# Kernel tuning notes

Measured on AMD Instinct MI355X. Metric: run time of the kernel, lower is better.

The kernel has to match this reference:

```python
import jax, jax.numpy as jnp
import numpy as np

N_CLASSES = 4
N_STEPS = 10
THRESHOLD = 0.7
ALPHA = 2.0


def _make_kernel_bias(n_classes, threshold):
    cross = np.zeros((3, 3, 3), dtype=np.float32)
    cross[1, 1, :] = 1.0
    cross[1, :, 1] = 1.0
    cross[:, 1, 1] = 1.0
    # depthwise kernel, OIDHW with I = 1 (groups = n_classes)
    kernel = (1.0 / 7.0 / (1.0 - threshold)) * np.tile(cross[None, None], (n_classes, 1, 1, 1, 1))
    bias = np.full((n_classes,), -threshold / (1.0 - threshold), dtype=np.float32)
    return jnp.asarray(kernel), jnp.asarray(bias)


def setup_inputs() -> dict:
    key = jax.random.key(0)
    k1, k2, k3 = jax.random.split(key, 3)
    B, C, D, H, W = 2, N_CLASSES, 128, 128, 128
    inp = jax.random.normal(k1, (B, C, D, H, W), dtype=jnp.float32)
    target = jax.random.randint(k2, (B, D, H, W), 0, C, dtype=jnp.int64)
    weight = jax.random.uniform(k3, (B, C), dtype=jnp.float32)
    kernel, bias = _make_kernel_bias(C, THRESHOLD)
    return {"input": inp, "target": target, "weight": weight, "kernel": kernel, "bias": bias}


def _erode(op, kernel, bias, n_classes):
    y = jax.lax.conv_general_dilated(
        op, kernel, window_strides=(1, 1, 1), padding=[(1, 1)] * 3,
        dimension_numbers=("NCDHW", "OIDHW", "NCDHW"),
        feature_group_count=n_classes)
    return jnp.maximum(y + bias[None, :, None, None, None], 0.0)


def reference(input, target, weight, kernel, bias):
    C = N_CLASSES
    probs = jax.nn.softmax(input, axis=1)
    # one_hot -> [B, D, H, W, C] -> [B, C, D, H, W]
    tgt = jnp.transpose(jax.nn.one_hot(target, C, dtype=probs.dtype), (0, 4, 1, 2, 3))
    op = jnp.square(probs - tgt)
    loss_t = jnp.zeros_like(op)
    for k in range(N_STEPS):
        op = _erode(op, kernel, bias, C)
        loss_t = loss_t + (float(k + 1) ** ALPHA) * op
    loss_t = loss_t * weight[:, :, None, None, None]
    return jnp.mean(loss_t)
```

## Files before the change

kernel.cpp:

```cpp
#include <hip/hip_runtime.h>

#define DHW   (128*128*128)
#define CDHW  (4*DHW)
#define NTOT  (2*CDHW)
#define NACC  1024

#define ROW4     32
#define IN_ROWS  12
#define S1_ROWS  10
#define IN_P4    (IN_ROWS*ROW4)
#define S1_P4    (S1_ROWS*ROW4)
#define SLOT4(z) (((z)+8)&3)
#define SLOT2(z) (((z)+8)&1)


__global__ __launch_bounds__(256, 4) void fused_sm_erode2_kernel(
    const float* __restrict__ in, const int* __restrict__ tgt,
    float4* __restrict__ dst,
    const float* __restrict__ kern, const float* __restrict__ bias,
    const float* __restrict__ weight, float c1, float c2,
    double* __restrict__ accs, int* __restrict__ flagOut)
{
    __shared__ float4 lin[4 * IN_P4];
    __shared__ float4 ls1[2 * S1_P4];
    __shared__ double wsum[4];
    __shared__ int    snz;

    const int tid = threadIdx.x;
    const int x  = blockIdx.x & 7;
    const int q  = blockIdx.x >> 3;
    const int c  = q & 3;
    const int t  = x * 32 + (q >> 2);
    const int y0 = (t & 15) << 3;
    const int zb = ((t >> 4) & 7) << 4;
    const int b  = (t >> 7) & 1;
    const int bc = b * 4 + c;
    const int fid = (bc << 7) | (((t >> 4) & 7) << 4) | (t & 15);

    const float4* in4 = (const float4*)in;
    const int4*   tg4 = (const int4*)tgt;
    const size_t  chb = ((size_t)(b * 4)) << 19;
    const size_t  co0 = chb + ((size_t)c << 19);
    const size_t  co1 = chb + ((size_t)((c + 1) & 3) << 19);
    const size_t  co2 = chb + ((size_t)((c + 2) & 3) << 19);
    const size_t  co3 = chb + ((size_t)((c + 3) & 3) << 19);
    float4*       dp  = dst + ((size_t)bc << 19);
    const float wk = kern[13];
    const float bs = bias[c];

    const int col  = tid & 31;
    const int trow = tid >> 5;

    if (tid == 0) snz = 0;

    const int  gy0  = y0 + trow - 2;
    const bool lv0  = ((unsigned)gy0 < 128u);
    const int  off0 = (lv0 ? gy0 : 0) * 32 + col;
    const bool act1 = (tid < 128);
    const int  gy1  = y0 + trow + 6;
    const bool lv1  = act1 && ((unsigned)gy1 < 128u);
    const int  off1 = (lv1 ? gy1 : 0) * 32 + col;

    const bool  sact1 = (tid < 64);
    const int   sr  = (tid < 32) ? 0 : 9;
    const float m1  = ((unsigned)(y0 + sr - 1) < 128u) ? 1.f : 0.f;
    const int   ci1 = (sr + 1) * 32 + (tid & 31);
    const int   so1 = sr * 32 + (tid & 31);

    const float lmask = (col == 0)  ? 0.f : 1.f;
    const float rmask = (col == 31) ? 0.f : 1.f;

    const int go4 = (y0 + trow) * 32 + col;

    const float4 f4z = make_float4(0.f, 0.f, 0.f, 0.f);
    float4 A00 = f4z, A01 = f4z, A02 = f4z, A03 = f4z;
    float4 A10 = f4z, A11 = f4z, A12 = f4z, A13 = f4z;
    int4   T0 = make_int4(0,0,0,0), T1 = make_int4(0,0,0,0);
    bool   ok0 = false, ok1 = false;
    float4 s_m = f4z, s_c = f4z, s_p = f4z;
    int    nz  = 0;

    auto prefetch = [&](int L) {
        const bool zok = ((unsigned)L < 128u);
        ok0 = zok && lv0;
        ok1 = zok && lv1;
        if (ok0) {
            size_t o = (size_t)(L << 12) + off0;
            A00 = in4[co0 + o];
            A01 = in4[co1 + o];
            A02 = in4[co2 + o];
            A03 = in4[co3 + o];
            T0  = tg4[((size_t)b << 19) + o];
        }
        if (ok1) {
            size_t o = (size_t)(L << 12) + off1;
            A10 = in4[co0 + o];
            A11 = in4[co1 + o];
            A12 = in4[co2 + o];
            A13 = in4[co3 + o];
            T1  = tg4[((size_t)b << 19) + o];
        }
    };
    auto op_one = [&](const float4& B0, const float4& B1, const float4& B2,
                      const float4& B3, const int4& T) -> float4 {
        float4 r;
        #define OP1(K)                                                         \
        {                                                                      \
            float vc = B0.K;                                                   \
            float sm = 1.0f + __expf(B1.K - vc) + __expf(B2.K - vc)            \
                            + __expf(B3.K - vc);                               \
            float d  = __builtin_amdgcn_rcpf(sm) - ((T.K == c) ? 1.0f : 0.0f); \
            r.K = d * d;                                                       \
        }
        OP1(x) OP1(y) OP1(z) OP1(w)
        #undef OP1
        return r;
    };
    auto commit = [&](int L) {
        float4* sl = lin + SLOT4(L) * IN_P4;
        float4 v0 = f4z, v1 = f4z;
        if (ok0) v0 = op_one(A00, A01, A02, A03, T0);
        if (ok1) v1 = op_one(A10, A11, A12, A13, T1);
        sl[tid] = v0;
        if (act1) sl[256 + tid] = v1;
    };
    auto s1one = [&](const float4* pzm, const float4* pzc, const float4* pzp,
                     int ci, float ym) -> float4 {
        float4 qC = pzc[ci];
        float4 qU = pzc[ci - 32];
        float4 qD = pzc[ci + 32];
        float4 qm = pzm[ci];
        float4 qp = pzp[ci];
        float lf = __shfl_up(qC.w, 1, 64)   * lmask;
        float rt = __shfl_down(qC.x, 1, 64) * rmask;
        float4 v;
        v.x = fmaxf((qC.x + lf   + qC.y + qU.x + qD.x + qm.x + qp.x) * wk + bs, 0.f) * ym;
        v.y = fmaxf((qC.y + qC.x + qC.z + qU.y + qD.y + qm.y + qp.y) * wk + bs, 0.f) * ym;
        v.z = fmaxf((qC.z + qC.y + qC.w + qU.z + qD.z + qm.z + qp.z) * wk + bs, 0.f) * ym;
        v.w = fmaxf((qC.w + qC.z + rt   + qU.w + qD.w + qm.w + qp.w) * wk + bs, 0.f) * ym;
        return v;
    };
    auto s1_phase = [&](int z) {
        float4* o = ls1 + SLOT2(z) * S1_P4;
        float4 vnew;
        if ((unsigned)z < 128u) {
            const float4* pzm = lin + SLOT4(z - 1) * IN_P4;
            const float4* pzc = lin + SLOT4(z)     * IN_P4;
            const float4* pzp = lin + SLOT4(z + 1) * IN_P4;
            vnew = s1one(pzm, pzc, pzp, tid + 64, 1.f);
            o[tid + 32] = vnew;
            if (sact1) o[so1] = s1one(pzm, pzc, pzp, ci1, m1);
        } else {
            vnew = f4z;
            o[tid + 32] = f4z;
            if (sact1) o[so1] = f4z;
        }
        s_m = s_c; s_c = s_p; s_p = vnew;
    };

    double part = 0.0;

    prefetch(zb - 2); commit(zb - 2);
    prefetch(zb - 1); commit(zb - 1);
    prefetch(zb);     commit(zb);
    prefetch(zb + 1);
    __syncthreads();
    s1_phase(zb - 1);

    for (int L = zb + 1; L <= zb + 17; ++L) {
        commit(L);
        __syncthreads();
        if (L <= zb + 16) prefetch(L + 1);
        s1_phase(L - 1);
        const int zo = L - 2;
        if (zo >= zb) {
            const float4* su = ls1 + SLOT2(zo) * S1_P4;
            float4 u4 = su[tid];
            float4 d4 = su[tid + 64];
            float lf = __shfl_up(s_c.w, 1, 64)   * lmask;
            float rt = __shfl_down(s_c.x, 1, 64) * rmask;
            float4 v;
            v.x = fmaxf((s_c.x + lf    + s_c.y + u4.x + d4.x + s_m.x + s_p.x) * wk + bs, 0.f);
            v.y = fmaxf((s_c.y + s_c.x + s_c.z + u4.y + d4.y + s_m.y + s_p.y) * wk + bs, 0.f);
            v.z = fmaxf((s_c.z + s_c.y + s_c.w + u4.z + d4.z + s_m.z + s_p.z) * wk + bs, 0.f);
            v.w = fmaxf((s_c.w + s_c.z + rt    + u4.w + d4.w + s_m.w + s_p.w) * wk + bs, 0.f);
            dp[((size_t)zo << 12) + go4] = v;
            nz |= (v.x != 0.f) | (v.y != 0.f) | (v.z != 0.f) | (v.w != 0.f);
            float pl = c1 * (s_c.x + s_c.y + s_c.z + s_c.w)
                     + c2 * (v.x   + v.y   + v.z   + v.w);
            part += (double)pl;
        }
    }

    #pragma unroll
    for (int off = 32; off > 0; off >>= 1)
        part += __shfl_down(part, off, 64);
    if ((tid & 63) == 0) wsum[tid >> 6] = part;
    if (__any(nz) && (tid & 63) == 0) atomicOr(&snz, 1);
    __syncthreads();
    if (tid == 0) {
        double tot = (wsum[0] + wsum[1] + wsum[2] + wsum[3]) * (double)weight[bc];
        accs[blockIdx.x] = tot;
        flagOut[fid] = snz;
    }
}

__global__ __launch_bounds__(256, 4) void erode2_kernel(
    const float4* __restrict__ src, float4* __restrict__ dst,
    const float* __restrict__ kern, const float* __restrict__ bias,
    const float* __restrict__ weight, float c1, float c2,
    int store, double* __restrict__ accs,
    const int* __restrict__ flagIn, int* __restrict__ flagOut)
{
    __shared__ float4 lin[4 * IN_P4];
    __shared__ float4 ls1[2 * S1_P4];
    __shared__ double wsum[4];
    __shared__ int    sf[9];
    __shared__ int    snz;

    const int tid = threadIdx.x;
    const int bid = ((blockIdx.x & 7) << 7) | (blockIdx.x >> 3);
    const int ty = bid & 15;
    const int tz = (bid >> 4) & 7;
    const int y0 = ty << 3;
    const int zb = tz << 4;
    const int bc = bid >> 7;

    if (tid < 9) {
        int dy = tid % 3 - 1, dz = tid / 3 - 1;
        int yt = ty + dy, zt = tz + dz;
        int f = 0;
        if ((unsigned)yt < 16u && (unsigned)zt < 8u)
            f = flagIn[(bc << 7) | (zt << 4) | yt];
        sf[tid] = f;
    }
    if (tid == 0) snz = 0;
    __syncthreads();
    const int any = sf[0] | sf[1] | sf[2] | sf[3] | sf[4]
                  | sf[5] | sf[6] | sf[7] | sf[8];
    if (!any) {
        if (tid == 0) {
            flagOut[bid] = 0;
        }
        return;
    }

    const float4* sp = src + ((size_t)bc << 19);
    float4*       dp = dst + ((size_t)bc << 19);
    const float wk = kern[13];
    const float bs = bias[bc & 3];

    const int col  = tid & 31;
    const int trow = tid >> 5;

    const int  gy0  = y0 + trow - 2;
    const bool lv0  = ((unsigned)gy0 < 128u);
    const int  off0 = (lv0 ? gy0 : 0) * 32 + col;
    const bool act1 = (tid < 128);
    const int  gy1  = y0 + trow + 6;
    const bool lv1  = act1 && ((unsigned)gy1 < 128u);
    const int  off1 = (lv1 ? gy1 : 0) * 32 + col;

    const int yd0 = (gy0 >> 3) - ty + 1;
    const int yd1 = (gy1 >> 3) - ty + 1;
    const int fmask0 = (sf[0 + ((unsigned)yd0 < 3u ? yd0 : 1)] ? 1 : 0)
                     | (sf[3 + ((unsigned)yd0 < 3u ? yd0 : 1)] ? 2 : 0)
                     | (sf[6 + ((unsigned)yd0 < 3u ? yd0 : 1)] ? 4 : 0);
    const int fmask1 = (sf[0 + ((unsigned)yd1 < 3u ? yd1 : 1)] ? 1 : 0)
                     | (sf[3 + ((unsigned)yd1 < 3u ? yd1 : 1)] ? 2 : 0)
                     | (sf[6 + ((unsigned)yd1 < 3u ? yd1 : 1)] ? 4 : 0);

    const bool  sact1 = (tid < 64);
    const int   sr  = (tid < 32) ? 0 : 9;
    const float m1  = ((unsigned)(y0 + sr - 1) < 128u) ? 1.f : 0.f;
    const int   ci1 = (sr + 1) * 32 + (tid & 31);
    const int   so1 = sr * 32 + (tid & 31);

    const float lmask = (col == 0)  ? 0.f : 1.f;
    const float rmask = (col == 31) ? 0.f : 1.f;

    const int go4 = (y0 + trow) * 32 + col;

    const float4 f4z = make_float4(0.f, 0.f, 0.f, 0.f);
    float4 pf0 = f4z, pf1 = f4z;
    float4 s_m = f4z, s_c = f4z, s_p = f4z;
    int    nz  = 0;

    auto prefetch = [&](int L) {
        pf0 = f4z; pf1 = f4z;
        if ((unsigned)L < 128u) {
            const int zidx = (L >> 4) - tz + 1;
            const float4* zp = sp + ((size_t)L << 12);
            if (lv0 && ((fmask0 >> zidx) & 1)) pf0 = zp[off0];
            if (lv1 && ((fmask1 >> zidx) & 1)) pf1 = zp[off1];
        }
    };
    auto commit = [&](int L) {
        float4* sl = lin + SLOT4(L) * IN_P4;
        sl[tid] = pf0;
        if (act1) sl[256 + tid] = pf1;
    };
    auto s1one = [&](const float4* pzm, const float4* pzc, const float4* pzp,
                     int ci, float ym) -> float4 {
        float4 qC = pzc[ci];
        float4 qU = pzc[ci - 32];
        float4 qD = pzc[ci + 32];
        float4 qm = pzm[ci];
        float4 qp = pzp[ci];
        float lf = __shfl_up(qC.w, 1, 64)   * lmask;
        float rt = __shfl_down(qC.x, 1, 64) * rmask;
        float4 v;
        v.x = fmaxf((qC.x + lf   + qC.y + qU.x + qD.x + qm.x + qp.x) * wk + bs, 0.f) * ym;
        v.y = fmaxf((qC.y + qC.x + qC.z + qU.y + qD.y + qm.y + qp.y) * wk + bs, 0.f) * ym;
        v.z = fmaxf((qC.z + qC.y + qC.w + qU.z + qD.z + qm.z + qp.z) * wk + bs, 0.f) * ym;
        v.w = fmaxf((qC.w + qC.z + rt   + qU.w + qD.w + qm.w + qp.w) * wk + bs, 0.f) * ym;
        return v;
    };
    auto s1_phase = [&](int z) {
        float4* o = ls1 + SLOT2(z) * S1_P4;
        float4 vnew;
        if ((unsigned)z < 128u) {
            const float4* pzm = lin + SLOT4(z - 1) * IN_P4;
            const float4* pzc = lin + SLOT4(z)     * IN_P4;
            const float4* pzp = lin + SLOT4(z + 1) * IN_P4;
            vnew = s1one(pzm, pzc, pzp, tid + 64, 1.f);
            o[tid + 32] = vnew;
            if (sact1) o[so1] = s1one(pzm, pzc, pzp, ci1, m1);
        } else {
            vnew = f4z;
            o[tid + 32] = f4z;
            if (sact1) o[so1] = f4z;
        }
        s_m = s_c; s_c = s_p; s_p = vnew;
    };

    double part = 0.0;

    prefetch(zb - 2); commit(zb - 2);
    prefetch(zb - 1); commit(zb - 1);
    prefetch(zb);     commit(zb);
    prefetch(zb + 1);
    __syncthreads();
    s1_phase(zb - 1);

    for (int L = zb + 1; L <= zb + 17; ++L) {
        commit(L);
        __syncthreads();
        if (L <= zb + 16) prefetch(L + 1);
        s1_phase(L - 1);
        const int zo = L - 2;
        if (zo >= zb) {
            const float4* su = ls1 + SLOT2(zo) * S1_P4;
            float4 u4 = su[tid];
            float4 d4 = su[tid + 64];
            float lf = __shfl_up(s_c.w, 1, 64)   * lmask;
            float rt = __shfl_down(s_c.x, 1, 64) * rmask;
            float4 v;
            v.x = fmaxf((s_c.x + lf    + s_c.y + u4.x + d4.x + s_m.x + s_p.x) * wk + bs, 0.f);
            v.y = fmaxf((s_c.y + s_c.x + s_c.z + u4.y + d4.y + s_m.y + s_p.y) * wk + bs, 0.f);
            v.z = fmaxf((s_c.z + s_c.y + s_c.w + u4.z + d4.z + s_m.z + s_p.z) * wk + bs, 0.f);
            v.w = fmaxf((s_c.w + s_c.z + rt    + u4.w + d4.w + s_m.w + s_p.w) * wk + bs, 0.f);
            if (store) dp[((size_t)zo << 12) + go4] = v;
            nz |= (v.x != 0.f) | (v.y != 0.f) | (v.z != 0.f) | (v.w != 0.f);
            float pl = c1 * (s_c.x + s_c.y + s_c.z + s_c.w)
                     + c2 * (v.x   + v.y   + v.z   + v.w);
            part += (double)pl;
        }
    }

    #pragma unroll
    for (int off = 32; off > 0; off >>= 1)
        part += __shfl_down(part, off, 64);
    if ((tid & 63) == 0) wsum[tid >> 6] = part;
    if (__any(nz) && (tid & 63) == 0) atomicOr(&snz, 1);
    __syncthreads();
    if (tid == 0) {
        flagOut[bid] = snz;
        double tot = (wsum[0] + wsum[1] + wsum[2] + wsum[3]) * (double)weight[bc];
        atomicAdd(&accs[bid], tot);
    }
}

__global__ __launch_bounds__(1024) void finalize_kernel(
    const double* __restrict__ accs, float* __restrict__ out)
{
    __shared__ double wsum[16];
    double v = accs[threadIdx.x];
    #pragma unroll
    for (int off = 32; off > 0; off >>= 1)
        v += __shfl_down(v, off, 64);
    int lane = threadIdx.x & 63;
    int wid  = threadIdx.x >> 6;
    if (lane == 0) wsum[wid] = v;
    __syncthreads();
    if (threadIdx.x == 0) {
        double tot = 0.0;
        #pragma unroll
        for (int i = 0; i < 16; ++i) tot += wsum[i];
        out[0] = (float)(tot / (double)NTOT);
    }
}

extern "C" void kernel_launch(void* const* d_in, const int* in_sizes, int n_in,
                              void* d_out, int out_size, void* d_ws, size_t ws_size,
                              hipStream_t stream) {
    const float* in     = (const float*)d_in[0];
    const int*   tgt    = (const int*)d_in[1];
    const float* weight = (const float*)d_in[2];
    const float* kern   = (const float*)d_in[3];
    const float* bias   = (const float*)d_in[4];
    float* out = (float*)d_out;

    char* ws = (char*)d_ws;
    float*  buf0   = (float*)ws;
    float*  buf1   = (float*)(ws + (size_t)NTOT * sizeof(float));
    double* accs   = (double*)(ws + (size_t)NTOT * 2 * sizeof(float));
    int*    flagsA = (int*)(ws + (size_t)NTOT * 2 * sizeof(float) + NACC * sizeof(double));
    int*    flagsB = flagsA + NACC;

    fused_sm_erode2_kernel<<<1024, 256, 0, stream>>>(
        in, tgt, (float4*)buf0, kern, bias, weight, 1.0f, 4.0f, accs, flagsA);

    float* cur = buf0;
    float* nxt = buf1;
    int*   fIn = flagsA;
    int*   fOut = flagsB;
    for (int p = 1; p < 5; ++p) {
        float c1 = (float)((2 * p + 1) * (2 * p + 1));
        float c2 = (float)((2 * p + 2) * (2 * p + 2));
        int   store = (p < 4) ? 1 : 0;
        erode2_kernel<<<1024, 256, 0, stream>>>(
            (const float4*)cur, (float4*)nxt, kern, bias, weight, c1, c2,
            store, accs, fIn, fOut);
        float* tb = cur; cur = nxt; nxt = tb;
        int*   tf = fIn; fIn = fOut; fOut = tf;
    }

    finalize_kernel<<<1, 1024, 0, stream>>>(accs, out);
}
```

Measured before the change: 163.6 us.

## Track per-z-slice nonzero flags to skip zero slice loads, compute and stores

Replaces the single per-tile nonzero flag with a 16-bit mask of z-slices that contain nonzero eroded values. Later erosion steps use the masks from neighbouring tiles to skip global loads, first-stage stencil work and second-stage compute for slices that must be zero. Stores are delayed by one iteration so that only slices voted nonzero get written. This adds per-slice ballot/atomic traffic and extra bit logic, and it relies on zero slices never being read back from stale memory.

```diff
diff --git a/kernel.cpp b/kernel.cpp
--- a/kernel.cpp
+++ b/kernel.cpp
@@ -24,7 +24,7 @@
     __shared__ float4 lin[4 * IN_P4];
     __shared__ float4 ls1[2 * S1_P4];
     __shared__ double wsum[4];
-    __shared__ int    snz;
+    __shared__ int    voteArr[16];
 
     const int tid = threadIdx.x;
     const int x  = blockIdx.x & 7;
@@ -51,7 +51,7 @@
     const int col  = tid & 31;
     const int trow = tid >> 5;
 
-    if (tid == 0) snz = 0;
+    if (tid < 16) voteArr[tid] = 0;
 
     const int  gy0  = y0 + trow - 2;
     const bool lv0  = ((unsigned)gy0 < 128u);
@@ -78,7 +78,7 @@
     int4   T0 = make_int4(0,0,0,0), T1 = make_int4(0,0,0,0);
     bool   ok0 = false, ok1 = false;
     float4 s_m = f4z, s_c = f4z, s_p = f4z;
-    int    nz  = 0;
+    float4 vH  = f4z;
 
     auto prefetch = [&](int L) {
         const bool zok = ((unsigned)L < 128u);
@@ -170,6 +170,9 @@
     for (int L = zb + 1; L <= zb + 17; ++L) {
         commit(L);
         __syncthreads();
+        const int zp = L - 3;
+        if (zp >= zb && voteArr[zp - zb] != 0)
+            dp[((size_t)zp << 12) + go4] = vH;
         if (L <= zb + 16) prefetch(L + 1);
         s1_phase(L - 1);
         const int zo = L - 2;
@@ -184,24 +187,30 @@
             v.y = fmaxf((s_c.y + s_c.x + s_c.z + u4.y + d4.y + s_m.y + s_p.y) * wk + bs, 0.f);
             v.z = fmaxf((s_c.z + s_c.y + s_c.w + u4.z + d4.z + s_m.z + s_p.z) * wk + bs, 0.f);
             v.w = fmaxf((s_c.w + s_c.z + rt    + u4.w + d4.w + s_m.w + s_p.w) * wk + bs, 0.f);
-            dp[((size_t)zo << 12) + go4] = v;
-            nz |= (v.x != 0.f) | (v.y != 0.f) | (v.z != 0.f) | (v.w != 0.f);
             float pl = c1 * (s_c.x + s_c.y + s_c.z + s_c.w)
                      + c2 * (v.x   + v.y   + v.z   + v.w);
             part += (double)pl;
-        }
-    }
+            bool nzv = (v.x != 0.f) || (v.y != 0.f) || (v.z != 0.f) || (v.w != 0.f);
+            if (__any(nzv) && (tid & 63) == 0) atomicOr(&voteArr[zo - zb], 1);
+            vH = v;
+        }
+    }
+
+    __syncthreads();
+    if (voteArr[15] != 0) dp[((size_t)(zb + 15) << 12) + go4] = vH;
 
     #pragma unroll
     for (int off = 32; off > 0; off >>= 1)
         part += __shfl_down(part, off, 64);
     if ((tid & 63) == 0) wsum[tid >> 6] = part;
-    if (__any(nz) && (tid & 63) == 0) atomicOr(&snz, 1);
     __syncthreads();
     if (tid == 0) {
+        int mask = 0;
+        #pragma unroll
+        for (int i = 0; i < 16; ++i) mask |= (voteArr[i] ? 1 : 0) << i;
+        flagOut[fid] = mask;
         double tot = (wsum[0] + wsum[1] + wsum[2] + wsum[3]) * (double)weight[bc];
         accs[blockIdx.x] = tot;
-        flagOut[fid] = snz;
     }
 }
 
@@ -216,7 +225,7 @@
     __shared__ float4 ls1[2 * S1_P4];
     __shared__ double wsum[4];
     __shared__ int    sf[9];
-    __shared__ int    snz;
+    __shared__ int    voteArr[16];
 
     const int tid = threadIdx.x;
     const int bid = ((blockIdx.x & 7) << 7) | (blockIdx.x >> 3);
@@ -234,16 +243,25 @@
             f = flagIn[(bc << 7) | (zt << 4) | yt];
         sf[tid] = f;
     }
-    if (tid == 0) snz = 0;
-    __syncthreads();
-    const int any = sf[0] | sf[1] | sf[2] | sf[3] | sf[4]
-                  | sf[5] | sf[6] | sf[7] | sf[8];
-    if (!any) {
-        if (tid == 0) {
-            flagOut[bid] = 0;
-        }
+    if (tid < 16) voteArr[tid] = 0;
+    __syncthreads();
+
+    unsigned aInW = 0;
+    #pragma unroll
+    for (int i = 0; i < 20; ++i) {
+        int L = zb - 2 + i;
+        if ((unsigned)L < 128u) {
+            int zi = (L >> 4) - tz + 1;
+            int m  = sf[zi * 3] | sf[zi * 3 + 1] | sf[zi * 3 + 2];
+            aInW |= (unsigned)((m >> (L & 15)) & 1) << i;
+        }
+    }
+    if (aInW == 0) {
+        if (tid == 0) flagOut[bid] = 0;
         return;
     }
+    const unsigned aS1W = aInW | (aInW << 1) | (aInW >> 1);
+    const unsigned aS2W = aS1W | (aS1W << 1) | (aS1W >> 1);
 
     const float4* sp = src + ((size_t)bc << 19);
     float4*       dp = dst + ((size_t)bc << 19);
@@ -261,14 +279,8 @@
     const bool lv1  = act1 && ((unsigned)gy1 < 128u);
     const int  off1 = (lv1 ? gy1 : 0) * 32 + col;
 
-    const int yd0 = (gy0 >> 3) - ty + 1;
-    const int yd1 = (gy1 >> 3) - ty + 1;
-    const int fmask0 = (sf[0 + ((unsigned)yd0 < 3u ? yd0 : 1)] ? 1 : 0)
-                     | (sf[3 + ((unsigned)yd0 < 3u ? yd0 : 1)] ? 2 : 0)
-                     | (sf[6 + ((unsigned)yd0 < 3u ? yd0 : 1)] ? 4 : 0);
-    const int fmask1 = (sf[0 + ((unsigned)yd1 < 3u ? yd1 : 1)] ? 1 : 0)
-                     | (sf[3 + ((unsigned)yd1 < 3u ? yd1 : 1)] ? 2 : 0)
-                     | (sf[6 + ((unsigned)yd1 < 3u ? yd1 : 1)] ? 4 : 0);
+    const int yd0c = (unsigned)((gy0 >> 3) - ty + 1) < 3u ? ((gy0 >> 3) - ty + 1) : 1;
+    const int yd1c = (unsigned)((gy1 >> 3) - ty + 1) < 3u ? ((gy1 >> 3) - ty + 1) : 1;
 
     const bool  sact1 = (tid < 64);
     const int   sr  = (tid < 32) ? 0 : 9;
@@ -284,15 +296,16 @@
     const float4 f4z = make_float4(0.f, 0.f, 0.f, 0.f);
     float4 pf0 = f4z, pf1 = f4z;
     float4 s_m = f4z, s_c = f4z, s_p = f4z;
-    int    nz  = 0;
+    float4 vH  = f4z;
 
     auto prefetch = [&](int L) {
         pf0 = f4z; pf1 = f4z;
         if ((unsigned)L < 128u) {
-            const int zidx = (L >> 4) - tz + 1;
+            const int zi = (L >> 4) - tz + 1;
+            const int sh = L & 15;
             const float4* zp = sp + ((size_t)L << 12);
-            if (lv0 && ((fmask0 >> zidx) & 1)) pf0 = zp[off0];
-            if (lv1 && ((fmask1 >> zidx) & 1)) pf1 = zp[off1];
+            if (lv0 && ((sf[zi * 3 + yd0c] >> sh) & 1)) pf0 = zp[off0];
+            if (lv1 && ((sf[zi * 3 + yd1c] >> sh) & 1)) pf1 = zp[off1];
         }
     };
     auto commit = [&](int L) {
@@ -317,19 +330,15 @@
         return v;
     };
     auto s1_phase = [&](int z) {
-        float4* o = ls1 + SLOT2(z) * S1_P4;
-        float4 vnew;
-        if ((unsigned)z < 128u) {
+        float4 vnew = f4z;
+        if ((unsigned)z < 128u && ((aS1W >> (z - zb + 2)) & 1)) {
+            float4* o = ls1 + SLOT2(z) * S1_P4;
             const float4* pzm = lin + SLOT4(z - 1) * IN_P4;
             const float4* pzc = lin + SLOT4(z)     * IN_P4;
             const float4* pzp = lin + SLOT4(z + 1) * IN_P4;
             vnew = s1one(pzm, pzc, pzp, tid + 64, 1.f);
             o[tid + 32] = vnew;
             if (sact1) o[so1] = s1one(pzm, pzc, pzp, ci1, m1);
-        } else {
-            vnew = f4z;
-            o[tid + 32] = f4z;
-            if (sact1) o[so1] = f4z;
         }
         s_m = s_c; s_c = s_p; s_p = vnew;
     };
@@ -346,36 +355,50 @@
     for (int L = zb + 1; L <= zb + 17; ++L) {
         commit(L);
         __syncthreads();
+        const int zp = L - 3;
+        if (store && zp >= zb && voteArr[zp - zb] != 0)
+            dp[((size_t)zp << 12) + go4] = vH;
         if (L <= zb + 16) prefetch(L + 1);
         s1_phase(L - 1);
         const int zo = L - 2;
         if (zo >= zb) {
-            const float4* su = ls1 + SLOT2(zo) * S1_P4;
-            float4 u4 = su[tid];
-            float4 d4 = su[tid + 64];
-            float lf = __shfl_up(s_c.w, 1, 64)   * lmask;
-            float rt = __shfl_down(s_c.x, 1, 64) * rmask;
-            float4 v;
-            v.x = fmaxf((s_c.x + lf    + s_c.y + u4.x + d4.x + s_m.x + s_p.x) * wk + bs, 0.f);
-            v.y = fmaxf((s_c.y + s_c.x + s_c.z + u4.y + d4.y + s_m.y + s_p.y) * wk + bs, 0.f);
-            v.z = fmaxf((s_c.z + s_c.y + s_c.w + u4.z + d4.z + s_m.z + s_p.z) * wk + bs, 0.f);
-            v.w = fmaxf((s_c.w + s_c.z + rt    + u4.w + d4.w + s_m.w + s_p.w) * wk + bs, 0.f);
-            if (store) dp[((size_t)zo << 12) + go4] = v;
-            nz |= (v.x != 0.f) | (v.y != 0.f) | (v.z != 0.f) | (v.w != 0.f);
-            float pl = c1 * (s_c.x + s_c.y + s_c.z + s_c.w)
-                     + c2 * (v.x   + v.y   + v.z   + v.w);
-            part += (double)pl;
-        }
-    }
+            float4 v = f4z;
+            if ((aS2W >> (zo - zb + 2)) & 1) {
+                float4 u4 = f4z, d4 = f4z;
+                if ((aS1W >> (zo - zb + 2)) & 1) {
+                    const float4* su = ls1 + SLOT2(zo) * S1_P4;
+                    u4 = su[tid];
+                    d4 = su[tid + 64];
+                }
+                float lf = __shfl_up(s_c.w, 1, 64)   * lmask;
+                float rt = __shfl_down(s_c.x, 1, 64) * rmask;
+                v.x = fmaxf((s_c.x + lf    + s_c.y + u4.x + d4.x + s_m.x + s_p.x) * wk + bs, 0.f);
+                v.y = fmaxf((s_c.y + s_c.x + s_c.z + u4.y + d4.y + s_m.y + s_p.y) * wk + bs, 0.f);
+                v.z = fmaxf((s_c.z + s_c.y + s_c.w + u4.z + d4.z + s_m.z + s_p.z) * wk + bs, 0.f);
+                v.w = fmaxf((s_c.w + s_c.z + rt    + u4.w + d4.w + s_m.w + s_p.w) * wk + bs, 0.f);
+                float pl = c1 * (s_c.x + s_c.y + s_c.z + s_c.w)
+                         + c2 * (v.x   + v.y   + v.z   + v.w);
+                part += (double)pl;
+                bool nzv = (v.x != 0.f) || (v.y != 0.f) || (v.z != 0.f) || (v.w != 0.f);
+                if (__any(nzv) && (tid & 63) == 0) atomicOr(&voteArr[zo - zb], 1);
+            }
+            vH = v;
+        }
+    }
+
+    __syncthreads();
+    if (store && voteArr[15] != 0) dp[((size_t)(zb + 15) << 12) + go4] = vH;
 
     #pragma unroll
     for (int off = 32; off > 0; off >>= 1)
         part += __shfl_down(part, off, 64);
     if ((tid & 63) == 0) wsum[tid >> 6] = part;
-    if (__any(nz) && (tid & 63) == 0) atomicOr(&snz, 1);
     __syncthreads();
     if (tid == 0) {
-        flagOut[bid] = snz;
+        int mask = 0;
+        #pragma unroll
+        for (int i = 0; i < 16; ++i) mask |= (voteArr[i] ? 1 : 0) << i;
+        flagOut[bid] = mask;
         double tot = (wsum[0] + wsum[1] + wsum[2] + wsum[3]) * (double)weight[bc];
         atomicAdd(&accs[bid], tot);
     }
```

Result: faster. 155.3 us (-5.0%).
